# Optimization experiments

Measured on AMD Instinct MI355X. Metric: run time of the kernel, lower is better.

Reference implementation:

```python
import jax, jax.numpy as jnp
import numpy as np

B, L1, L2 = 8, 512, 512
FULL, HID, NLVL = 2048, 1024, 8
D = HID // NLVL  # attsize_per_lvl


def setup_inputs() -> dict:
    key = jax.random.key(0)
    k1, k2, k3, k4, k5, k6 = jax.random.split(key, 6)
    x1_att = jax.random.normal(k1, (B, L1, FULL), dtype=jnp.float32)
    x2_att = jax.random.normal(k2, (B, L2, FULL), dtype=jnp.float32)
    x2 = jax.random.normal(k3, (B, L2, HID), dtype=jnp.float32)
    x2_mask = jax.random.randint(k4, (B, L2), 0, 2).astype(bool)
    # nn.Linear(full_size, hidden_size, bias=False): weight [HID, FULL]
    W = jax.random.normal(k5, (HID, FULL), dtype=jnp.float32) / np.sqrt(FULL)
    final_v = jnp.ones((HID,), dtype=jnp.float32)  # linear_final param
    return {"x1_att": x1_att, "x2_att": x2_att, "x2": x2, "x2_mask": x2_mask,
            "W": W, "final_v": final_v}


def reference(x1_att, x2_att, x2, x2_mask, W, final_v):
    # dropout is identity in eval mode
    x1_key = jax.nn.relu(jnp.einsum('blf,hf->blh', x1_att, W))            # [B,L1,HID]
    x2_key = final_v * jax.nn.relu(jnp.einsum('blf,hf->blh', x2_att, W))  # [B,L2,HID]
    x1_rep = x1_key.reshape(B, L1, NLVL, D)  # split hidden into levels
    x2_rep = x2_key.reshape(B, L2, NLVL, D)
    scores = jnp.einsum('bqnd,bknd->bnqk', x1_rep, x2_rep)  # [B,NLVL,L1,L2]
    scores = jnp.where(x2_mask[:, None, None, :], -jnp.inf, scores)
    alpha = jax.nn.softmax(scores, axis=-1)                 # softmax over len2
    x2_lvl = x2.reshape(B, L2, NLVL, D)                     # value split per level
    atten = jnp.einsum('bnqk,bknd->bqnd', alpha, x2_lvl)    # [B,L1,NLVL,D]
    return atten.reshape(B, L1, HID)
```

## Files before the change

### kernel.cpp

```cpp
#include <hip/hip_runtime.h>
#include <stdint.h>

typedef _Float16 f16;
typedef _Float16 f16x4 __attribute__((ext_vector_type(4)));
typedef _Float16 f16x8 __attribute__((ext_vector_type(8)));
typedef float f32x4 __attribute__((ext_vector_type(4)));
typedef float f32x16 __attribute__((ext_vector_type(16)));

typedef const __attribute__((address_space(1))) void* gas_ptr;
typedef __attribute__((address_space(3))) void* las_ptr;

__device__ __forceinline__ void gload16(const void* g, void* l) {
  __builtin_amdgcn_global_load_lds((gas_ptr)g, (las_ptr)l, 16, 0, 0);
}

#define OFF_A16 0u
#define OFF_W16 33554432u
#define OFF_K16 37748736u
#define OFF_VT  54525952u
#define WS_NEED 62914560u

__global__ void k_convert(const float* __restrict__ x1a, const float* __restrict__ x2a,
                          const float* __restrict__ W, f16* __restrict__ A16,
                          f16* __restrict__ W16) {
  const int NA = (8192 * 2048) / 4;
  const int NH = NA / 2;
  const int NW = (1024 * 2048) / 4;
  const int NT = NA + NW;
  for (int g = blockIdx.x * blockDim.x + threadIdx.x; g < NT; g += gridDim.x * blockDim.x) {
    if (g < NA) {
      const float* src = (g < NH) ? (x1a + 4 * (size_t)g) : (x2a + 4 * (size_t)(g - NH));
      float4 v = *(const float4*)src;
      f16x4 h; h[0] = (f16)v.x; h[1] = (f16)v.y; h[2] = (f16)v.z; h[3] = (f16)v.w;
      *((f16x4*)A16 + g) = h;
    } else {
      int gw = g - NA;
      float4 v = *((const float4*)W + gw);
      f16x4 h; h[0] = (f16)v.x; h[1] = (f16)v.y; h[2] = (f16)v.z; h[3] = (f16)v.w;
      *((f16x4*)W16 + gw) = h;
    }
  }
}

__global__ void k_transpose_v(const float* __restrict__ x2, f16* __restrict__ VT) {
  __shared__ f16 T[128 * 130];
  int bid = blockIdx.x;
  int kt = bid & 3, n = (bid >> 2) & 7, b = bid >> 5;
  int t = threadIdx.x;
  int k0 = kt * 128;
  #pragma unroll
  for (int p = 0; p < 16; ++p) {
    int kl = p * 8 + (t >> 5);
    int c4 = t & 31;
    float4 v = *(const float4*)(x2 + (size_t)(b * 512 + k0 + kl) * 1024 + n * 128 + c4 * 4);
    int d0 = c4 * 4;
    T[(d0 + 0) * 130 + kl] = (f16)v.x;
    T[(d0 + 1) * 130 + kl] = (f16)v.y;
    T[(d0 + 2) * 130 + kl] = (f16)v.z;
    T[(d0 + 3) * 130 + kl] = (f16)v.w;
  }
  __syncthreads();
  #pragma unroll
  for (int p = 0; p < 8; ++p) {
    int d = p * 16 + (t >> 4);
    int c = t & 15;
    f16x8 h;
    #pragma unroll
    for (int j = 0; j < 8; ++j) h[j] = T[d * 130 + c * 8 + j];
    *(f16x8*)(VT + (size_t)((b * 8 + n) * 128 + d) * 512 + k0 + c * 8) = h;
  }
}

__global__ void __launch_bounds__(256)
k_gemm_keys(const f16* __restrict__ A16, const f16* __restrict__ W16,
            const float* __restrict__ final_v, f16* __restrict__ K16) {
  __shared__ f16 Alds[128 * 128];
  __shared__ f16 Wlds[128 * 128];
  int bid = blockIdx.x;
  int sw = (bid & 7) * 64 + (bid >> 3);
  int mt = sw >> 3, nt = sw & 7;
  int t = threadIdx.x, l = t & 63, w = t >> 6;
  int wm = w >> 1, wn = w & 1;
  f32x16 acc[2][2];
  #pragma unroll
  for (int i = 0; i < 2; ++i)
    #pragma unroll
    for (int j = 0; j < 2; ++j)
      #pragma unroll
      for (int r = 0; r < 16; ++r) acc[i][j][r] = 0.f;
  const char* Ab = (const char*)A16 + (size_t)mt * 128 * 4096;
  const char* Wb = (const char*)W16 + (size_t)nt * 128 * 4096;
  size_t soff[8];
  #pragma unroll
  for (int i = 0; i < 8; ++i) {
    int row = (w * 8 + i) * 4 + (l >> 4);
    soff[i] = (size_t)row * 4096 + (((l & 15) ^ (row & 15)) << 4);
  }
  int g8 = l >> 5;
  int rowA = wm * 64 + (l & 31);
  int rowB = wn * 64 + (l & 31);
  int sA = rowA & 15, sB = rowB & 15;
  const char* rdA0 = (const char*)Alds + rowA * 256;
  const char* rdB0 = (const char*)Wlds + rowB * 256;
  for (int ks = 0; ks < 16; ++ks) {
    int k0b = ks * 256;
    #pragma unroll
    for (int i = 0; i < 8; ++i) {
      gload16(Ab + soff[i] + k0b, (char*)Alds + (w * 8 + i) * 1024);
      gload16(Wb + soff[i] + k0b, (char*)Wlds + (w * 8 + i) * 1024);
    }
    __syncthreads();
    f16x8 af[2][8], bf[2][8];
    #pragma unroll
    for (int mi = 0; mi < 2; ++mi)
      #pragma unroll
      for (int ks2 = 0; ks2 < 8; ++ks2) {
        af[mi][ks2] = *(const f16x8*)(rdA0 + mi * 8192 + (((ks2 * 2 + g8) ^ sA) << 4));
        bf[mi][ks2] = *(const f16x8*)(rdB0 + mi * 8192 + (((ks2 * 2 + g8) ^ sB) << 4));
      }
    #pragma unroll
    for (int ks2 = 0; ks2 < 8; ++ks2)
      #pragma unroll
      for (int mi = 0; mi < 2; ++mi)
        #pragma unroll
        for (int ni = 0; ni < 2; ++ni)
          acc[mi][ni] = __builtin_amdgcn_mfma_f32_32x32x16_f16(af[mi][ks2], bf[ni][ks2], acc[mi][ni], 0, 0, 0);
    __syncthreads();
  }
  bool isx2 = (mt >= 32);
  int c = l & 31, r2 = l >> 5;
  #pragma unroll
  for (int ni = 0; ni < 2; ++ni) {
    int col = nt * 128 + wn * 64 + ni * 32 + c;
    float fvv = isx2 ? final_v[col] : 1.0f;
    #pragma unroll
    for (int mi = 0; mi < 2; ++mi) {
      int rowbase = mt * 128 + wm * 64 + mi * 32 + 4 * r2;
      #pragma unroll
      for (int r = 0; r < 16; ++r) {
        int row = rowbase + (r & 3) + 8 * (r >> 2);
        K16[(size_t)row * 1024 + col] = (f16)(fmaxf(acc[mi][ni][r], 0.f) * fvv);
      }
    }
  }
}

__global__ void __launch_bounds__(256)
k_attn(const f16* __restrict__ K16, const f16* __restrict__ VT,
       const int* __restrict__ mask, float* __restrict__ out) {
  __shared__ f16 Klds[2 * 64 * 128];
  __shared__ f16 Vlds[2 * 128 * 64];
  __shared__ f16 Plds[4 * 16 * 64];
  __shared__ float bias[512];
  int bid = blockIdx.x;
  int qt = bid & 7, n = (bid >> 3) & 7, b = bid >> 6;
  int t = threadIdx.x, l = t & 63, w = t >> 6;
  for (int i = t; i < 512; i += 256) bias[i] = mask[b * 512 + i] ? -1e30f : 0.0f;
  int r4 = l >> 4;
  int slot = (l & 15) << 4;
  int lg = r4 << 4;
  const char* Kg = (const char*)K16 + ((size_t)(4096 + b * 512) * 1024 + n * 128) * 2;
  const char* Vg = (const char*)VT + (size_t)((b * 8 + n) * 128) * 1024;
  int vr = l >> 3;
  int vslot = (l & 7) << 4;

#define STAGE_KV(ktv, bufsel) do {                                              \
    _Pragma("unroll")                                                           \
    for (int i_ = 0; i_ < 4; ++i_) {                                            \
      int rl_ = w * 16 + i_ * 4 + r4;                                           \
      gload16(Kg + (size_t)((ktv) * 64 + rl_) * 2048 + (slot ^ ((rl_ & 7) << 4)), \
              (char*)Klds + (bufsel) * 16384 + (w * 16 + i_ * 4) * 256);        \
    }                                                                           \
    _Pragma("unroll")                                                           \
    for (int i_ = 0; i_ < 4; ++i_) {                                            \
      int dl_ = w * 32 + i_ * 8 + vr;                                           \
      gload16(Vg + (size_t)dl_ * 1024 + (ktv) * 128 + (vslot ^ ((dl_ & 7) << 4)), \
              (char*)Vlds + (bufsel) * 16384 + (w * 32 + i_ * 8) * 128);        \
    }                                                                           \
  } while (0)

  const char* Qg = (const char*)K16 + ((size_t)(b * 512 + qt * 64) * 1024 + n * 128) * 2;
  int qrow = w * 16 + (l & 15);
  f16x8 qf[4];
  #pragma unroll
  for (int kk = 0; kk < 4; ++kk)
    qf[kk] = *(const f16x8*)(Qg + (size_t)qrow * 2048 + kk * 64 + lg);
  f32x4 o[8];
  #pragma unroll
  for (int dt = 0; dt < 8; ++dt) { o[dt][0] = 0.f; o[dt][1] = 0.f; o[dt][2] = 0.f; o[dt][3] = 0.f; }
  float m_r[4], l_r[4];
  #pragma unroll
  for (int r = 0; r < 4; ++r) { m_r[r] = -1e30f; l_r[r] = 0.0f; }
  char* Pw = (char*)Plds + w * 2048;

  STAGE_KV(0, 0);
  __syncthreads();
  #pragma unroll 8
  for (int kt = 0; kt < 8; ++kt) {
    int cur = kt & 1;
    if (kt < 7) STAGE_KV(kt + 1, cur ^ 1);
    const char* Kl = (const char*)Klds + cur * 16384;
    const char* Vl = (const char*)Vlds + cur * 16384;
    f32x4 s[4];
    #pragma unroll
    for (int nt4 = 0; nt4 < 4; ++nt4) {
      s[nt4][0] = 0.f; s[nt4][1] = 0.f; s[nt4][2] = 0.f; s[nt4][3] = 0.f;
      int krow = nt4 * 16 + (l & 15);
      int ksz = (krow & 7) << 4;
      #pragma unroll
      for (int kk = 0; kk < 4; ++kk) {
        f16x8 kf = *(const f16x8*)(Kl + krow * 256 + ((kk * 64 + lg) ^ ksz));
        s[nt4] = __builtin_amdgcn_mfma_f32_16x16x32_f16(qf[kk], kf, s[nt4], 0, 0, 0);
      }
      float bc = bias[kt * 64 + nt4 * 16 + (l & 15)];
      #pragma unroll
      for (int r = 0; r < 4; ++r) s[nt4][r] += bc;
    }
    float pmax[4], scale[4], csum[4];
    #pragma unroll
    for (int r = 0; r < 4; ++r)
      pmax[r] = fmaxf(fmaxf(s[0][r], s[1][r]), fmaxf(s[2][r], s[3][r]));
    #pragma unroll
    for (int off = 1; off <= 8; off <<= 1) {
      #pragma unroll
      for (int r = 0; r < 4; ++r) pmax[r] = fmaxf(pmax[r], __shfl_xor(pmax[r], off));
    }
    #pragma unroll
    for (int r = 0; r < 4; ++r) {
      float mn = fmaxf(m_r[r], pmax[r]);
      scale[r] = __expf(m_r[r] - mn);
      m_r[r] = mn;
      csum[r] = 0.0f;
    }
    #pragma unroll
    for (int nt4 = 0; nt4 < 4; ++nt4) {
      #pragma unroll
      for (int r = 0; r < 4; ++r) {
        float sv = s[nt4][r];
        float p = (sv <= -1e29f) ? 0.0f : __expf(sv - m_r[r]);
        csum[r] += p;
        int prow = (r4 << 2) + r;
        int addr = prow * 128 + (((nt4 * 16 + (l & 15)) * 2) ^ ((prow & 7) << 4));
        *(f16*)(Pw + addr) = (f16)p;
      }
    }
    #pragma unroll
    for (int off = 1; off <= 8; off <<= 1) {
      #pragma unroll
      for (int r = 0; r < 4; ++r) csum[r] += __shfl_xor(csum[r], off);
    }
    #pragma unroll
    for (int r = 0; r < 4; ++r) l_r[r] = l_r[r] * scale[r] + csum[r];
    #pragma unroll
    for (int dt = 0; dt < 8; ++dt) {
      #pragma unroll
      for (int r = 0; r < 4; ++r) o[dt][r] *= scale[r];
    }
    asm volatile("s_waitcnt lgkmcnt(0)" ::: "memory");
    int prow = l & 15;
    int psz = (prow & 7) << 4;
    f16x8 pf0 = *(const f16x8*)((const char*)Pw + prow * 128 + (lg ^ psz));
    f16x8 pf1 = *(const f16x8*)((const char*)Pw + prow * 128 + ((lg + 64) ^ psz));
    #pragma unroll
    for (int dt = 0; dt < 8; ++dt) {
      int drow = dt * 16 + (l & 15);
      int dsz = (drow & 7) << 4;
      f16x8 vf0 = *(const f16x8*)(Vl + drow * 128 + (lg ^ dsz));
      f16x8 vf1 = *(const f16x8*)(Vl + drow * 128 + ((lg + 64) ^ dsz));
      o[dt] = __builtin_amdgcn_mfma_f32_16x16x32_f16(pf0, vf0, o[dt], 0, 0, 0);
      o[dt] = __builtin_amdgcn_mfma_f32_16x16x32_f16(pf1, vf1, o[dt], 0, 0, 0);
    }
    __syncthreads();
  }
#undef STAGE_KV
  size_t ob = (size_t)(b * 512 + qt * 64 + w * 16 + (r4 << 2)) * 1024 + n * 128 + (l & 15);
  #pragma unroll
  for (int r = 0; r < 4; ++r) {
    float inv = 1.0f / fmaxf(l_r[r], 1e-30f);
    #pragma unroll
    for (int dt = 0; dt < 8; ++dt)
      out[ob + (size_t)r * 1024 + dt * 16] = o[dt][r] * inv;
  }
}

extern "C" void kernel_launch(void* const* d_in, const int* in_sizes, int n_in,
                              void* d_out, int out_size, void* d_ws, size_t ws_size,
                              hipStream_t stream) {
  const float* x1a = (const float*)d_in[0];
  const float* x2a = (const float*)d_in[1];
  const float* x2  = (const float*)d_in[2];
  const int*   msk = (const int*)d_in[3];
  const float* W   = (const float*)d_in[4];
  const float* fv  = (const float*)d_in[5];
  float* out = (float*)d_out;
  if (ws_size < (size_t)WS_NEED) return;
  char* ws = (char*)d_ws;
  f16* A16 = (f16*)(ws + OFF_A16);
  f16* W16 = (f16*)(ws + OFF_W16);
  f16* K16 = (f16*)(ws + OFF_K16);
  f16* VT  = (f16*)(ws + OFF_VT);
  k_convert<<<2048, 256, 0, stream>>>(x1a, x2a, W, A16, W16);
  k_transpose_v<<<256, 256, 0, stream>>>(x2, VT);
  k_gemm_keys<<<512, 256, 0, stream>>>(A16, W16, fv, K16);
  k_attn<<<512, 256, 0, stream>>>(K16, VT, msk, out);
}
```

Measured before the change: 96.55 us.

## Fuse fp32-to-fp16 conversion into key GEMM, dropping separate convert pass

Removes the standalone conversion kernel that wrote fp16 copies of x1_att, x2_att and W to workspace. The key GEMM now streams fp32 tiles straight into LDS via global_load_lds and converts them to fp16 in registers before the MFMAs. This avoids one full read and write of the large activation tensors and a kernel launch. In exchange the GEMM moves twice as many bytes per K step, runs twice as many K iterations with half the K depth per tile, and does extra conversion ALU work in the inner loop.

```diff
diff --git a/kernel.cpp b/kernel.cpp
--- a/kernel.cpp
+++ b/kernel.cpp
@@ -14,33 +14,9 @@
   __builtin_amdgcn_global_load_lds((gas_ptr)g, (las_ptr)l, 16, 0, 0);
 }
 
-#define OFF_A16 0u
-#define OFF_W16 33554432u
-#define OFF_K16 37748736u
-#define OFF_VT  54525952u
-#define WS_NEED 62914560u
-
-__global__ void k_convert(const float* __restrict__ x1a, const float* __restrict__ x2a,
-                          const float* __restrict__ W, f16* __restrict__ A16,
-                          f16* __restrict__ W16) {
-  const int NA = (8192 * 2048) / 4;
-  const int NH = NA / 2;
-  const int NW = (1024 * 2048) / 4;
-  const int NT = NA + NW;
-  for (int g = blockIdx.x * blockDim.x + threadIdx.x; g < NT; g += gridDim.x * blockDim.x) {
-    if (g < NA) {
-      const float* src = (g < NH) ? (x1a + 4 * (size_t)g) : (x2a + 4 * (size_t)(g - NH));
-      float4 v = *(const float4*)src;
-      f16x4 h; h[0] = (f16)v.x; h[1] = (f16)v.y; h[2] = (f16)v.z; h[3] = (f16)v.w;
-      *((f16x4*)A16 + g) = h;
-    } else {
-      int gw = g - NA;
-      float4 v = *((const float4*)W + gw);
-      f16x4 h; h[0] = (f16)v.x; h[1] = (f16)v.y; h[2] = (f16)v.z; h[3] = (f16)v.w;
-      *((f16x4*)W16 + gw) = h;
-    }
-  }
-}
+#define OFF_K16 0u
+#define OFF_VT  16777216u
+#define WS_NEED 25165824u
 
 __global__ void k_transpose_v(const float* __restrict__ x2, f16* __restrict__ VT) {
   __shared__ f16 T[128 * 130];
@@ -72,10 +48,11 @@
 }
 
 __global__ void __launch_bounds__(256)
-k_gemm_keys(const f16* __restrict__ A16, const f16* __restrict__ W16,
-            const float* __restrict__ final_v, f16* __restrict__ K16) {
-  __shared__ f16 Alds[128 * 128];
-  __shared__ f16 Wlds[128 * 128];
+k_gemm_keys(const float* __restrict__ x1a, const float* __restrict__ x2a,
+            const float* __restrict__ Wf, const float* __restrict__ final_v,
+            f16* __restrict__ K16) {
+  __shared__ float Alds[128 * 64];
+  __shared__ float Wlds[128 * 64];
   int bid = blockIdx.x;
   int sw = (bid & 7) * 64 + (bid >> 3);
   int mt = sw >> 3, nt = sw & 7;
@@ -88,21 +65,21 @@
     for (int j = 0; j < 2; ++j)
       #pragma unroll
       for (int r = 0; r < 16; ++r) acc[i][j][r] = 0.f;
-  const char* Ab = (const char*)A16 + (size_t)mt * 128 * 4096;
-  const char* Wb = (const char*)W16 + (size_t)nt * 128 * 4096;
+  bool isx2 = (mt >= 32);
+  const char* Ab = (const char*)(isx2 ? (x2a + (size_t)(mt - 32) * 128 * 2048)
+                                      : (x1a + (size_t)mt * 128 * 2048));
+  const char* Wb = (const char*)(Wf + (size_t)nt * 128 * 2048);
   size_t soff[8];
   #pragma unroll
   for (int i = 0; i < 8; ++i) {
     int row = (w * 8 + i) * 4 + (l >> 4);
-    soff[i] = (size_t)row * 4096 + (((l & 15) ^ (row & 15)) << 4);
+    soff[i] = (size_t)row * 8192 + (((l & 15) ^ (row & 15)) << 4);
   }
   int g8 = l >> 5;
-  int rowA = wm * 64 + (l & 31);
-  int rowB = wn * 64 + (l & 31);
-  int sA = rowA & 15, sB = rowB & 15;
-  const char* rdA0 = (const char*)Alds + rowA * 256;
-  const char* rdB0 = (const char*)Wlds + rowB * 256;
-  for (int ks = 0; ks < 16; ++ks) {
+  int sxy = l & 15;
+  const char* rdA0 = (const char*)Alds + (wm * 64 + (l & 31)) * 256;
+  const char* rdB0 = (const char*)Wlds + (wn * 64 + (l & 31)) * 256;
+  for (int ks = 0; ks < 32; ++ks) {
     int k0b = ks * 256;
     #pragma unroll
     for (int i = 0; i < 8; ++i) {
@@ -110,16 +87,29 @@
       gload16(Wb + soff[i] + k0b, (char*)Wlds + (w * 8 + i) * 1024);
     }
     __syncthreads();
-    f16x8 af[2][8], bf[2][8];
-    #pragma unroll
-    for (int mi = 0; mi < 2; ++mi)
-      #pragma unroll
-      for (int ks2 = 0; ks2 < 8; ++ks2) {
-        af[mi][ks2] = *(const f16x8*)(rdA0 + mi * 8192 + (((ks2 * 2 + g8) ^ sA) << 4));
-        bf[mi][ks2] = *(const f16x8*)(rdB0 + mi * 8192 + (((ks2 * 2 + g8) ^ sB) << 4));
-      }
-    #pragma unroll
-    for (int ks2 = 0; ks2 < 8; ++ks2)
+    f16x8 af[2][4], bf[2][4];
+    #pragma unroll
+    for (int mi = 0; mi < 2; ++mi) {
+      const char* pa = rdA0 + mi * 8192;
+      const char* pb = rdB0 + mi * 8192;
+      #pragma unroll
+      for (int ks2 = 0; ks2 < 4; ++ks2) {
+        int s0 = ks2 * 4 + g8 * 2;
+        f32x4 alo = *(const f32x4*)(pa + ((s0 ^ sxy) << 4));
+        f32x4 ahi = *(const f32x4*)(pa + (((s0 + 1) ^ sxy) << 4));
+        f32x4 blo = *(const f32x4*)(pb + ((s0 ^ sxy) << 4));
+        f32x4 bhi = *(const f32x4*)(pb + (((s0 + 1) ^ sxy) << 4));
+        f16x8 ta, tb;
+        #pragma unroll
+        for (int j = 0; j < 4; ++j) {
+          ta[j] = (f16)alo[j]; ta[4 + j] = (f16)ahi[j];
+          tb[j] = (f16)blo[j]; tb[4 + j] = (f16)bhi[j];
+        }
+        af[mi][ks2] = ta; bf[mi][ks2] = tb;
+      }
+    }
+    #pragma unroll
+    for (int ks2 = 0; ks2 < 4; ++ks2)
       #pragma unroll
       for (int mi = 0; mi < 2; ++mi)
         #pragma unroll
@@ -127,7 +117,6 @@
           acc[mi][ni] = __builtin_amdgcn_mfma_f32_32x32x16_f16(af[mi][ks2], bf[ni][ks2], acc[mi][ni], 0, 0, 0);
     __syncthreads();
   }
-  bool isx2 = (mt >= 32);
   int c = l & 31, r2 = l >> 5;
   #pragma unroll
   for (int ni = 0; ni < 2; ++ni) {
@@ -295,12 +284,9 @@
   float* out = (float*)d_out;
   if (ws_size < (size_t)WS_NEED) return;
   char* ws = (char*)d_ws;
-  f16* A16 = (f16*)(ws + OFF_A16);
-  f16* W16 = (f16*)(ws + OFF_W16);
   f16* K16 = (f16*)(ws + OFF_K16);
   f16* VT  = (f16*)(ws + OFF_VT);
-  k_convert<<<2048, 256, 0, stream>>>(x1a, x2a, W, A16, W16);
   k_transpose_v<<<256, 256, 0, stream>>>(x2, VT);
-  k_gemm_keys<<<512, 256, 0, stream>>>(A16, W16, fv, K16);
+  k_gemm_keys<<<512, 256, 0, stream>>>(x1a, x2a, W, fv, K16);
   k_attn<<<512, 256, 0, stream>>>(K16, VT, msk, out);
 }
```

Result: no change. 97.34 us (+0.8%).
